# Kernel tuning notes

Measured on AMD Instinct MI355X. Metric: run time of the kernel, lower is better.

## Reference

```python
import jax, jax.numpy as jnp
import numpy as np

N_HEAD = 16

def setup_inputs() -> dict:
    key = jax.random.key(0)
    ks = jax.random.split(key, 4)
    C = 2048
    x = jax.random.normal(ks[0], (4, 2048, C), dtype=jnp.float32)
    # weights stored [in, out] (transpose of torch Linear's [out, in]); same math y = x @ W + b
    w_qkv = jax.random.normal(ks[1], (C, 3 * C), dtype=jnp.float32) * (1.0 / np.sqrt(C))
    b_qkv = jnp.zeros((3 * C,), dtype=jnp.float32)
    w_proj = jax.random.normal(ks[2], (C, C), dtype=jnp.float32) * (1.0 / np.sqrt(C))
    b_proj = jnp.zeros((C,), dtype=jnp.float32)
    return {"x": x, "w_qkv": w_qkv, "b_qkv": b_qkv, "w_proj": w_proj, "b_proj": b_proj}

def reference(x, w_qkv, b_qkv, w_proj, b_proj):
    B, S, C = x.shape
    H = N_HEAD
    D = C // H
    qkv = x @ w_qkv + b_qkv                      # [B,S,3C]
    q, k, v = jnp.split(qkv, 3, axis=-1)
    # [B,H,S,D]
    q = q.reshape(B, S, H, D).transpose(0, 2, 1, 3)
    k = k.reshape(B, S, H, D).transpose(0, 2, 1, 3)
    v = v.reshape(B, S, H, D).transpose(0, 2, 1, 3)
    scale = 1.0 / np.sqrt(D).astype(np.float32)
    scores = jnp.einsum('bhqd,bhkd->bhqk', q, k) * scale   # [B,H,S,S]
    causal = jnp.tril(jnp.ones((S, S), dtype=bool))
    scores = jnp.where(causal, scores, jnp.finfo(scores.dtype).min)
    attn = jax.nn.softmax(scores, axis=-1)
    y = jnp.einsum('bhqk,bhkd->bhqd', attn, v)              # [B,H,S,D]
    y = y.transpose(0, 2, 1, 3).reshape(B, S, C)
    return y @ w_proj + b_proj
```

## Files before the change

kernel.cpp:

```cpp
#include <hip/hip_runtime.h>
#include <hip/hip_bf16.h>

typedef __bf16 bf16x8 __attribute__((ext_vector_type(8)));
typedef float floatx4 __attribute__((ext_vector_type(4)));

__device__ __forceinline__ unsigned short f2bf(float f) {
  unsigned u = __float_as_uint(f);
  u += 0x7fffu + ((u >> 16) & 1u);
  return (unsigned short)(u >> 16);
}

__device__ __forceinline__ unsigned cvt_pk_bf16(float lo, float hi) {
  unsigned r;
  asm("v_cvt_pk_bf16_f32 %0, %1, %2" : "=v"(r) : "v"(lo), "v"(hi));
  return r;
}

__device__ __forceinline__ void async_copy16(const void* g, void* l) {
  __builtin_amdgcn_global_load_lds(
      (const __attribute__((address_space(1))) void*)g,
      (__attribute__((address_space(3))) void*)l, 16, 0, 0);
}

__global__ __launch_bounds__(256) void cvt_bf16(
    const float* __restrict__ in, unsigned short* __restrict__ out) {
  size_t i = ((size_t)blockIdx.x * 256 + threadIdx.x) * 8;
  float4 a0 = *(const float4*)&in[i];
  float4 a1 = *(const float4*)&in[i + 4];
  uint4 d;
  d.x = (unsigned)f2bf(a0.x) | ((unsigned)f2bf(a0.y) << 16);
  d.y = (unsigned)f2bf(a0.z) | ((unsigned)f2bf(a0.w) << 16);
  d.z = (unsigned)f2bf(a1.x) | ((unsigned)f2bf(a1.y) << 16);
  d.w = (unsigned)f2bf(a1.z) | ((unsigned)f2bf(a1.w) << 16);
  *(uint4*)(&out[i]) = d;
}

__global__ __launch_bounds__(256) void transpose_cvt(
    const float* __restrict__ in, unsigned short* __restrict__ out,
    int R, int Ccol) {
  __shared__ unsigned short tile[32][33];
  int c0 = blockIdx.x * 32, r0 = blockIdx.y * 32;
  int tx = threadIdx.x & 31, ty = threadIdx.x >> 5;
  #pragma unroll
  for (int i = 0; i < 32; i += 8)
    tile[ty + i][tx] = f2bf(in[(size_t)(r0 + ty + i) * Ccol + c0 + tx]);
  __syncthreads();
  #pragma unroll
  for (int i = 0; i < 32; i += 8)
    out[(size_t)(c0 + ty + i) * R + r0 + tx] = tile[tx][ty + i];
}

__device__ __forceinline__ void stage_chunk256(
    const unsigned short* __restrict__ A, const unsigned short* __restrict__ Bt,
    int K, int m0, int n0, int k0,
    unsigned short* As, unsigned short* Bs, int lane, int w, int j) {
  const int lrow = lane >> 3;
  const int gch = (lane & 7) ^ lrow;
  if (j < 2) {
    #pragma unroll
    for (int u = 2 * j; u < 2 * j + 2; u++) {
      int g = w * 4 + u;
      int row = g * 8 + lrow;
      async_copy16(&A[(size_t)(m0 + row) * K + k0 + gch * 8], &As[g * 512]);
    }
  } else {
    #pragma unroll
    for (int u = 2 * (j - 2); u < 2 * (j - 2) + 2; u++) {
      int g = w * 4 + u;
      int row = g * 8 + lrow;
      async_copy16(&Bt[(size_t)(n0 + row) * K + k0 + gch * 8], &Bs[g * 512]);
    }
  }
}

__device__ __forceinline__ void gemm_bt_256(
    const unsigned short* __restrict__ A, const unsigned short* __restrict__ Bt,
    int K, int m0, int n0,
    unsigned short* AsB, unsigned short* BsB,
    floatx4 acc[8][4]) {
  const int t = threadIdx.x, lane = t & 63, w = t >> 6;
  const int wr = w >> 2, wc = w & 3;
  const int l15 = lane & 15, l4 = lane >> 4;
  const floatx4 zf = {0.f, 0.f, 0.f, 0.f};
  #pragma unroll
  for (int mi = 0; mi < 8; mi++)
    #pragma unroll
    for (int ni = 0; ni < 4; ni++) acc[mi][ni] = zf;

  const int nkt = K >> 6;
  #pragma unroll
  for (int j = 0; j < 4; j++)
    stage_chunk256(A, Bt, K, m0, n0, 0, AsB, BsB, lane, w, j);

  #pragma unroll 1
  for (int kt = 0; kt < nkt; kt++) {
    const unsigned short* Ab = AsB + (kt & 1) * 16384;
    const unsigned short* Bb = BsB + (kt & 1) * 16384;
    unsigned short* An = AsB + ((kt + 1) & 1) * 16384;
    unsigned short* Bn = BsB + ((kt + 1) & 1) * 16384;
    const bool pf = (kt + 1 < nkt);
    if (pf) {
      stage_chunk256(A, Bt, K, m0, n0, (kt + 1) * 64, An, Bn, lane, w, 0);
      asm volatile("s_waitcnt vmcnt(2)" ::: "memory");
    } else {
      asm volatile("s_waitcnt vmcnt(0)" ::: "memory");
    }
    __builtin_amdgcn_s_barrier();
    #pragma unroll
    for (int j = 0; j < 4; j++) {
      const int qm = j >> 1, qn = j & 1;
      bf16x8 af[4][2], bfr[2][2];
      #pragma unroll
      for (int mi = 0; mi < 4; mi++) {
        int row = wr * 128 + (qm * 4 + mi) * 16 + l15;
        #pragma unroll
        for (int kk = 0; kk < 2; kk++)
          af[mi][kk] = *(const bf16x8*)(
              &Ab[row * 64 + (((kk * 4 + l4) ^ (l15 & 7)) << 3)]);
      }
      #pragma unroll
      for (int ni = 0; ni < 2; ni++) {
        int row = wc * 64 + (qn * 2 + ni) * 16 + l15;
        #pragma unroll
        for (int kk = 0; kk < 2; kk++)
          bfr[ni][kk] = *(const bf16x8*)(
              &Bb[row * 64 + (((kk * 4 + l4) ^ (l15 & 7)) << 3)]);
      }
      if (j < 3 && pf)
        stage_chunk256(A, Bt, K, m0, n0, (kt + 1) * 64, An, Bn, lane, w, j + 1);
      __builtin_amdgcn_s_barrier();
      __builtin_amdgcn_s_setprio(1);
      #pragma unroll
      for (int kk = 0; kk < 2; kk++)
        #pragma unroll
        for (int mi = 0; mi < 4; mi++)
          #pragma unroll
          for (int ni = 0; ni < 2; ni++)
            acc[qm * 4 + mi][qn * 2 + ni] = __builtin_amdgcn_mfma_f32_16x16x32_bf16(
                af[mi][kk], bfr[ni][kk], acc[qm * 4 + mi][qn * 2 + ni], 0, 0, 0);
      __builtin_amdgcn_s_setprio(0);
      if (j < 3) __builtin_amdgcn_s_barrier();
    }
  }
  __builtin_amdgcn_s_barrier();
}

__global__ __launch_bounds__(512, 2) void gemm_qkv(
    const unsigned short* __restrict__ X, const unsigned short* __restrict__ WT,
    const float* __restrict__ bias,
    unsigned short* __restrict__ Qo, unsigned short* __restrict__ Ko,
    unsigned short* __restrict__ Vto) {
  __shared__ unsigned short As[2][256 * 64];
  __shared__ unsigned short Bs[2][256 * 64];
  int lg = blockIdx.x;
  int bn = lg % 24, bm = lg / 24;
  int m0 = bm * 256, n0 = bn * 256;
  floatx4 acc[8][4];
  gemm_bt_256(X, WT, 2048, m0, n0, As[0], Bs[0], acc);

  const int t = threadIdx.x, lane = t & 63, w = t >> 6;
  const int wr = w >> 2, wc = w & 3;
  const int l15 = lane & 15, l4 = lane >> 4;
  int which = n0 >> 11;
  int b = m0 >> 11;
  int s0 = m0 & 2047;
  float bv[4];
  #pragma unroll
  for (int ni = 0; ni < 4; ni++)
    bv[ni] = bias[n0 + wc * 64 + ni * 16 + l15];

  if (which < 2) {
    unsigned short* dst = (which == 0) ? Qo : Ko;
    #pragma unroll
    for (int ni = 0; ni < 4; ni++) {
      int cn = (n0 & 2047) + wc * 64 + ni * 16;
      int h = cn >> 7, d = (cn & 127) + l15;
      size_t base = ((size_t)(b * 16 + h)) * 2048;
      #pragma unroll
      for (int mi = 0; mi < 8; mi++) {
        #pragma unroll
        for (int r = 0; r < 4; r++) {
          int srow = s0 + wr * 128 + mi * 16 + l4 * 4 + r;
          dst[(base + srow) * 128 + d] = f2bf(acc[mi][ni][r] + bv[ni]);
        }
      }
    }
  } else {
    #pragma unroll
    for (int ni = 0; ni < 4; ni++) {
      int cn = (n0 & 2047) + wc * 64 + ni * 16;
      int h = cn >> 7, d = (cn & 127) + l15;
      #pragma unroll
      for (int mi = 0; mi < 8; mi++) {
        int sr = s0 + wr * 128 + mi * 16 + l4 * 4;
        ushort4 v;
        v.x = f2bf(acc[mi][ni][0] + bv[ni]);
        v.y = f2bf(acc[mi][ni][1] + bv[ni]);
        v.z = f2bf(acc[mi][ni][2] + bv[ni]);
        v.w = f2bf(acc[mi][ni][3] + bv[ni]);
        *(ushort4*)(&Vto[((size_t)(b * 16 + h) * 128 + d) * 2048 + sr]) = v;
      }
    }
  }
}

__device__ __forceinline__ void attn_stage(
    const unsigned short* __restrict__ Kb, const unsigned short* __restrict__ Vb,
    __bf16* Ksel, __bf16* Vsel, int k0, int lane, int w) {
  const int krow_in = lane >> 4, kch = lane & 15;
  const int vrow_in = lane >> 3, vch = lane & 7;
  #pragma unroll
  for (int u = 0; u < 2; u++) {
    int uk = w * 2 + u;
    int row = uk * 4 + krow_in;
    int sch = kch ^ (row & 7);
    async_copy16(&Kb[(size_t)(k0 + row) * 128 + sch * 8], Ksel + uk * 512);
  }
  #pragma unroll
  for (int u = 0; u < 2; u++) {
    int uv = w * 2 + u;
    int row = uv * 8 + vrow_in;
    int sch = vch ^ vrow_in;
    async_copy16(&Vb[(size_t)row * 2048 + k0 + sch * 8], Vsel + uv * 512);
  }
}

__global__ __launch_bounds__(512, 4) void attn(
    const unsigned short* __restrict__ Qg, const unsigned short* __restrict__ Kg,
    const unsigned short* __restrict__ Vtg, unsigned short* __restrict__ Yg) {
  const int S = 2048, Dh = 128;
  const float c1 = 0.08838834764831845f * 1.4426950408889634f;
  const float NEG_BIG = -3.0e38f;
  __shared__ __bf16 Ks[2][64 * 128];
  __shared__ __bf16 Vs[2][128 * 64];
  __shared__ __bf16 Ps[8][16 * 64];

  int wg = blockIdx.x;
  int lg = (wg & 7) * 64 + (wg >> 3);
  int qtp = lg & 7;
  int bh = lg >> 3;
  const int t = threadIdx.x, lane = t & 63, w = t >> 6;
  const int l15 = lane & 15, l4 = lane >> 4;
  const unsigned short* Qb = Qg + (size_t)bh * S * Dh;
  const unsigned short* Kb = Kg + (size_t)bh * S * Dh;
  const unsigned short* Vb = Vtg + (size_t)bh * Dh * S;
  __bf16* Pw = Ps[w];
  int b = bh >> 4, h = bh & 15;
  const floatx4 zf = {0.f, 0.f, 0.f, 0.f};

  #pragma unroll 1
  for (int half = 0; half < 2; half++) {
    int jq = half ? qtp : (15 - qtp);
    int qb0 = jq * 128;
    int qrow_base = qb0 + w * 16;
    bf16x8 qf[4];
    #pragma unroll
    for (int kk = 0; kk < 4; kk++)
      qf[kk] = *(const bf16x8*)(
          &Qb[(size_t)(qrow_base + l15) * Dh + kk * 32 + l4 * 8]);
    floatx4 accO[8];
    #pragma unroll
    for (int nd = 0; nd < 8; nd++) accO[nd] = zf;
    float mst = NEG_BIG, lst = 0.f;

    int ntiles = 2 * jq + 2;
    int cur = 0;
    attn_stage(Kb, Vb, Ks[0], Vs[0], 0, lane, w);
    __syncthreads();

    #pragma unroll 1
    for (int kt = 0; kt < ntiles; kt++) {
      if (kt + 1 < ntiles)
        attn_stage(Kb, Vb, Ks[cur ^ 1], Vs[cur ^ 1], (kt + 1) * 64, lane, w);

      const __bf16* Kcur = Ks[cur];
      const __bf16* Vcur = Vs[cur];
      floatx4 sc[4];
      #pragma unroll
      for (int ni = 0; ni < 4; ni++) sc[ni] = zf;
      __builtin_amdgcn_s_setprio(1);
      #pragma unroll
      for (int kk = 0; kk < 4; kk++) {
        bf16x8 kf[4];
        #pragma unroll
        for (int ni = 0; ni < 4; ni++) {
          int row = ni * 16 + l15;
          kf[ni] = *(const bf16x8*)(
              &Kcur[row * 128 + (((kk * 4 + l4) ^ (l15 & 7)) << 3)]);
        }
        #pragma unroll
        for (int ni = 0; ni < 4; ni++)
          sc[ni] = __builtin_amdgcn_mfma_f32_16x16x32_bf16(kf[ni], qf[kk], sc[ni], 0, 0, 0);
      }
      __builtin_amdgcn_s_setprio(0);

      if (kt >= 2 * jq) {
        int kb = kt * 64 - qb0 - w * 16 - l15;
        #pragma unroll
        for (int ni = 0; ni < 4; ni++)
          #pragma unroll
          for (int r = 0; r < 4; r++)
            if (kb + ni * 16 + l4 * 4 + r > 0) sc[ni][r] = NEG_BIG;
      }

      float mt = fmaxf(fmaxf(fmaxf(sc[0][0], sc[0][1]), fmaxf(sc[0][2], sc[0][3])),
                       fmaxf(fmaxf(sc[1][0], sc[1][1]), fmaxf(sc[1][2], sc[1][3])));
      mt = fmaxf(mt,
           fmaxf(fmaxf(fmaxf(sc[2][0], sc[2][1]), fmaxf(sc[2][2], sc[2][3])),
                 fmaxf(fmaxf(sc[3][0], sc[3][1]), fmaxf(sc[3][2], sc[3][3]))));
      mt = fmaxf(mt, __shfl_xor(mt, 16, 64));
      mt = fmaxf(mt, __shfl_xor(mt, 32, 64));

      if (!__all(mt <= mst + 8.0f)) {
        float mnew = fmaxf(mst, mt);
        float alpha = exp2f((mst - mnew) * c1);
        mst = mnew;
        lst *= alpha;
        float ar[4];
        #pragma unroll
        for (int r = 0; r < 4; r++)
          ar[r] = __shfl(alpha, l4 * 20 + r, 64);
        #pragma unroll
        for (int nd = 0; nd < 8; nd++)
          #pragma unroll
          for (int r = 0; r < 4; r++) accO[nd][r] *= ar[r];
      }

      float mc = mst * c1;
      float p[4][4];
      float rs = 0.f;
      #pragma unroll
      for (int ni = 0; ni < 4; ni++)
        #pragma unroll
        for (int r = 0; r < 4; r++) {
          p[ni][r] = exp2f(sc[ni][r] * c1 - mc);
          rs += p[ni][r];
        }
      rs += __shfl_xor(rs, 16, 64);
      rs += __shfl_xor(rs, 32, 64);
      lst += rs;

      #pragma unroll
      for (int ni = 0; ni < 4; ni++) {
        uint2 dw;
        dw.x = cvt_pk_bf16(p[ni][0], p[ni][1]);
        dw.y = cvt_pk_bf16(p[ni][2], p[ni][3]);
        int s = ni * 4 + l4;
        *(uint2*)(&Pw[l15 * 64 + (((s >> 1) ^ (l15 & 7)) << 3) + ((s & 1) << 2)]) = dw;
      }

      __builtin_amdgcn_s_setprio(1);
      #pragma unroll
      for (int kk = 0; kk < 2; kk++) {
        bf16x8 pf = *(const bf16x8*)(
            &Pw[l15 * 64 + (((kk * 4 + l4) ^ (l15 & 7)) << 3)]);
        #pragma unroll
        for (int nd = 0; nd < 8; nd++) {
          int row = nd * 16 + l15;
          bf16x8 vf = *(const bf16x8*)(
              &Vcur[row * 64 + (((kk * 4 + l4) ^ (l15 & 7)) << 3)]);
          accO[nd] = __builtin_amdgcn_mfma_f32_16x16x32_bf16(pf, vf, accO[nd], 0, 0, 0);
        }
      }
      __builtin_amdgcn_s_setprio(0);
      __syncthreads();
      cur ^= 1;
    }

    float invl = 1.0f / lst;
    float ivr[4];
    #pragma unroll
    for (int r = 0; r < 4; r++)
      ivr[r] = __shfl(invl, l4 * 20 + r, 64);
    #pragma unroll
    for (int r = 0; r < 4; r++) {
      int srow = qrow_base + l4 * 4 + r;
      size_t rowbase = ((size_t)(b * 2048 + srow)) * 2048 + h * 128;
      #pragma unroll
      for (int nd = 0; nd < 8; nd++)
        Yg[rowbase + nd * 16 + l15] = f2bf(accO[nd][r] * ivr[r]);
    }
  }
}

__global__ __launch_bounds__(512, 2) void gemm_proj(
    const unsigned short* __restrict__ Yin, const unsigned short* __restrict__ WT,
    const float* __restrict__ bias, float* __restrict__ Og) {
  __shared__ unsigned short As[2][256 * 64];
  __shared__ unsigned short Bs[2][256 * 64];
  int lg = blockIdx.x;
  int bn = lg % 8, bm = lg / 8;
  int m0 = bm * 256, n0 = bn * 256;
  floatx4 acc[8][4];
  gemm_bt_256(Yin, WT, 2048, m0, n0, As[0], Bs[0], acc);

  const int t = threadIdx.x, lane = t & 63, w = t >> 6;
  const int wr = w >> 2, wc = w & 3;
  const int l15 = lane & 15, l4 = lane >> 4;
  float bv[4];
  #pragma unroll
  for (int ni = 0; ni < 4; ni++)
    bv[ni] = bias[n0 + wc * 64 + ni * 16 + l15];
  #pragma unroll
  for (int mi = 0; mi < 8; mi++)
    #pragma unroll
    for (int ni = 0; ni < 4; ni++)
      #pragma unroll
      for (int r = 0; r < 4; r++)
        Og[(size_t)(m0 + wr * 128 + mi * 16 + l4 * 4 + r) * 2048 +
           n0 + wc * 64 + ni * 16 + l15] = acc[mi][ni][r] + bv[ni];
}

extern "C" void kernel_launch(void* const* d_in, const int* in_sizes, int n_in,
                              void* d_out, int out_size, void* d_ws, size_t ws_size,
                              hipStream_t stream) {
  const float* x      = (const float*)d_in[0];
  const float* w_qkv  = (const float*)d_in[1];
  const float* b_qkv  = (const float*)d_in[2];
  const float* w_proj = (const float*)d_in[3];
  const float* b_proj = (const float*)d_in[4];
  float* out = (float*)d_out;
  char* ws = (char*)d_ws;

  unsigned short* Q   = (unsigned short*)d_out;
  unsigned short* Kt  = (unsigned short*)((char*)d_out + 33554432);
  unsigned short* Vt  = (unsigned short*)(ws);
  unsigned short* Xbf = (unsigned short*)(ws + 33554432);
  unsigned short* Y   = (unsigned short*)(ws + 33554432);
  unsigned short* WqT = (unsigned short*)(ws + 67108864);
  unsigned short* WpT = (unsigned short*)(ws + 67108864);

  cvt_bf16<<<dim3(8192), 256, 0, stream>>>(x, Xbf);
  transpose_cvt<<<dim3(192, 64), 256, 0, stream>>>(w_qkv, WqT, 2048, 6144);
  gemm_qkv<<<dim3(768), 512, 0, stream>>>(Xbf, WqT, b_qkv, Q, Kt, Vt);
  attn<<<dim3(512), 512, 0, stream>>>(Q, Kt, Vt, Y);
  transpose_cvt<<<dim3(64, 64), 256, 0, stream>>>(w_proj, WpT, 2048, 2048);
  gemm_proj<<<dim3(256), 512, 0, stream>>>(Y, WpT, b_proj, out);
}
```

Measured before the change: 590.0 us.

## Restructure 256x256 GEMM main loop into two k-substeps with whole-tile prefetch

```diff
diff --git a/kernel.cpp b/kernel.cpp
--- a/kernel.cpp
+++ b/kernel.cpp
@@ -50,26 +50,16 @@
     out[(size_t)(c0 + ty + i) * R + r0 + tx] = tile[tx][ty + i];
 }
 
-__device__ __forceinline__ void stage_chunk256(
-    const unsigned short* __restrict__ A, const unsigned short* __restrict__ Bt,
-    int K, int m0, int n0, int k0,
-    unsigned short* As, unsigned short* Bs, int lane, int w, int j) {
+__device__ __forceinline__ void stage_rows256(
+    const unsigned short* __restrict__ P, int K, int r0, int k0,
+    unsigned short* Ls, int lane, int w) {
   const int lrow = lane >> 3;
   const int gch = (lane & 7) ^ lrow;
-  if (j < 2) {
-    #pragma unroll
-    for (int u = 2 * j; u < 2 * j + 2; u++) {
-      int g = w * 4 + u;
-      int row = g * 8 + lrow;
-      async_copy16(&A[(size_t)(m0 + row) * K + k0 + gch * 8], &As[g * 512]);
-    }
-  } else {
-    #pragma unroll
-    for (int u = 2 * (j - 2); u < 2 * (j - 2) + 2; u++) {
-      int g = w * 4 + u;
-      int row = g * 8 + lrow;
-      async_copy16(&Bt[(size_t)(n0 + row) * K + k0 + gch * 8], &Bs[g * 512]);
-    }
+  #pragma unroll
+  for (int u = 0; u < 4; u++) {
+    int g = w * 4 + u;
+    int row = g * 8 + lrow;
+    async_copy16(&P[(size_t)(r0 + row) * K + k0 + gch * 8], &Ls[g * 512]);
   }
 }
 
@@ -88,9 +78,8 @@
     for (int ni = 0; ni < 4; ni++) acc[mi][ni] = zf;
 
   const int nkt = K >> 6;
-  #pragma unroll
-  for (int j = 0; j < 4; j++)
-    stage_chunk256(A, Bt, K, m0, n0, 0, AsB, BsB, lane, w, j);
+  stage_rows256(A, K, m0, 0, AsB, lane, w);
+  stage_rows256(Bt, K, n0, 0, BsB, lane, w);
 
   #pragma unroll 1
   for (int kt = 0; kt < nkt; kt++) {
@@ -100,49 +89,41 @@
     unsigned short* Bn = BsB + ((kt + 1) & 1) * 16384;
     const bool pf = (kt + 1 < nkt);
     if (pf) {
-      stage_chunk256(A, Bt, K, m0, n0, (kt + 1) * 64, An, Bn, lane, w, 0);
-      asm volatile("s_waitcnt vmcnt(2)" ::: "memory");
+      stage_rows256(A, K, m0, (kt + 1) * 64, An, lane, w);
+      asm volatile("s_waitcnt vmcnt(4)" ::: "memory");
     } else {
       asm volatile("s_waitcnt vmcnt(0)" ::: "memory");
     }
     __builtin_amdgcn_s_barrier();
     #pragma unroll
-    for (int j = 0; j < 4; j++) {
-      const int qm = j >> 1, qn = j & 1;
-      bf16x8 af[4][2], bfr[2][2];
-      #pragma unroll
-      for (int mi = 0; mi < 4; mi++) {
-        int row = wr * 128 + (qm * 4 + mi) * 16 + l15;
-        #pragma unroll
-        for (int kk = 0; kk < 2; kk++)
-          af[mi][kk] = *(const bf16x8*)(
-              &Ab[row * 64 + (((kk * 4 + l4) ^ (l15 & 7)) << 3)]);
-      }
-      #pragma unroll
-      for (int ni = 0; ni < 2; ni++) {
-        int row = wc * 64 + (qn * 2 + ni) * 16 + l15;
-        #pragma unroll
-        for (int kk = 0; kk < 2; kk++)
-          bfr[ni][kk] = *(const bf16x8*)(
-              &Bb[row * 64 + (((kk * 4 + l4) ^ (l15 & 7)) << 3)]);
-      }
-      if (j < 3 && pf)
-        stage_chunk256(A, Bt, K, m0, n0, (kt + 1) * 64, An, Bn, lane, w, j + 1);
+    for (int kk = 0; kk < 2; kk++) {
+      bf16x8 af[8], bfr[4];
+      #pragma unroll
+      for (int mi = 0; mi < 8; mi++) {
+        int row = wr * 128 + mi * 16 + l15;
+        af[mi] = *(const bf16x8*)(
+            &Ab[row * 64 + (((kk * 4 + l4) ^ (l15 & 7)) << 3)]);
+      }
+      #pragma unroll
+      for (int ni = 0; ni < 4; ni++) {
+        int row = wc * 64 + ni * 16 + l15;
+        bfr[ni] = *(const bf16x8*)(
+            &Bb[row * 64 + (((kk * 4 + l4) ^ (l15 & 7)) << 3)]);
+      }
+      if (kk == 0 && pf)
+        stage_rows256(Bt, K, n0, (kt + 1) * 64, Bn, lane, w);
       __builtin_amdgcn_s_barrier();
       __builtin_amdgcn_s_setprio(1);
       #pragma unroll
-      for (int kk = 0; kk < 2; kk++)
-        #pragma unroll
-        for (int mi = 0; mi < 4; mi++)
-          #pragma unroll
-          for (int ni = 0; ni < 2; ni++)
-            acc[qm * 4 + mi][qn * 2 + ni] = __builtin_amdgcn_mfma_f32_16x16x32_bf16(
-                af[mi][kk], bfr[ni][kk], acc[qm * 4 + mi][qn * 2 + ni], 0, 0, 0);
+      for (int mi = 0; mi < 8; mi++)
+        #pragma unroll
+        for (int ni = 0; ni < 4; ni++)
+          acc[mi][ni] = __builtin_amdgcn_mfma_f32_16x16x32_bf16(
+              af[mi], bfr[ni], acc[mi][ni], 0, 0, 0);
       __builtin_amdgcn_s_setprio(0);
-      if (j < 3) __builtin_amdgcn_s_barrier();
-    }
-  }
-  __builtin_amdgcn_s_barrier();
+      __builtin_amdgcn_s_barrier();
+    }
+  }
 }
 
 __global__ __launch_bounds__(512, 2) void gemm_qkv(
```

Result: faster. 569.0 us (-3.6%).
